# Optimization experiments

Measured on AMD Instinct MI355X. Metric: run time of the kernel, lower is better.

## Reference

```python
import jax, jax.numpy as jnp
import numpy as np

N, E, D, H = 16000, 256000, 128, 4
ALPHA = 0.2  # LeakyReLU negative slope


def setup_inputs() -> dict:
    key = jax.random.key(0)
    ks = jax.random.split(key, 9)
    s = 0.1
    return {
        "h": jax.random.normal(ks[0], (N, D), jnp.float32),
        "W": jax.random.normal(ks[1], (H, D, D), jnp.float32) * s,
        "a": jax.random.normal(ks[2], (H, 2 * D), jnp.float32) * s,
        "W_ih": jax.random.normal(ks[3], (3 * D, H * D), jnp.float32) * s,
        "W_hh": jax.random.normal(ks[4], (3 * D, D), jnp.float32) * s,
        "b_ih": jnp.zeros((3 * D,), jnp.float32),
        "b_hh": jnp.zeros((3 * D,), jnp.float32),
        "src": jax.random.randint(ks[5], (E,), 0, N, jnp.int32),
        "dst": jax.random.randint(ks[6], (E,), 0, N, jnp.int32),
    }


def reference(h, W, a, W_ih, W_hh, b_ih, b_hh, src, dst):
    n = h.shape[0]
    # Per-head linear transform: Wh[n,h,d]
    Wh = jnp.einsum("nd,hde->nhe", h, W)
    a1, a2 = a[:, :D], a[:, D:]
    s_src = jnp.einsum("nhd,hd->nh", Wh, a1)  # src attention logits
    s_dst = jnp.einsum("nhd,hd->nh", Wh, a2)  # dst attention logits
    e = jax.nn.leaky_relu(s_src[src] + s_dst[dst], ALPHA)  # [E,H]
    # Segment softmax over incoming edges of each dst node
    m = jax.ops.segment_max(e, dst, num_segments=n)          # [N,H]
    ex = jnp.exp(e - m[dst])
    denom = jax.ops.segment_sum(ex, dst, num_segments=n)     # [N,H]
    att = ex / denom[dst]                                    # [E,H]
    # Weighted message aggregation: h_prime[n,h,d]
    h_prime = jax.ops.segment_sum(att[:, :, None] * Wh[src], dst, num_segments=n)
    x = h_prime.reshape(n, H * D)  # concat heads
    # PyTorch GRUCell(input=H*D, hidden=D)
    gi = x @ W_ih.T + b_ih
    gh = h @ W_hh.T + b_hh
    i_r, i_z, i_n = jnp.split(gi, 3, axis=1)
    h_r, h_z, h_n = jnp.split(gh, 3, axis=1)
    r = jax.nn.sigmoid(i_r + h_r)
    z = jax.nn.sigmoid(i_z + h_z)
    nvec = jnp.tanh(i_n + r * h_n)
    return (1.0 - z) * nvec + z * h
```

## Files before the change

### kernel.cpp

```cpp
#include <hip/hip_runtime.h>
#include <math.h>

#define N_NODES 16000
#define E_EDGES 256000
#define DIM 128
#define HEADS 4
#define LRELU_ALPHA 0.2f
#define SLOT 64

typedef unsigned short u16;
typedef unsigned int u32;
typedef short bf16x8 __attribute__((ext_vector_type(8)));
typedef float floatx4 __attribute__((ext_vector_type(4)));

#define AS1 __attribute__((address_space(1)))
#define AS3 __attribute__((address_space(3)))

__device__ __forceinline__ u16 f2bf(float f) {
    u32 u = __float_as_uint(f);
    u32 r = (u + 0x7fffu + ((u >> 16) & 1u)) >> 16;
    return (u16)r;
}
__device__ __forceinline__ float bflo(u32 v) { return __uint_as_float(v << 16); }
__device__ __forceinline__ float bfhi(u32 v) { return __uint_as_float(v & 0xffff0000u); }
__device__ __forceinline__ float bfs(u16 v) { return __uint_as_float((u32)v << 16); }
__device__ __forceinline__ u32 pack2(float lo, float hi) {
    return (u32)f2bf(lo) | ((u32)f2bf(hi) << 16);
}


__device__ __forceinline__ void mt_tile(const float* __restrict__ W_ih,
    const float* __restrict__ W, u16* __restrict__ Wcat, int y, int z, char* SMp, int tid)
{
    u16 (*Alds)[32] = (u16(*)[32])SMp;
    u16 (*Blds)[32] = (u16(*)[32])(SMp + 8192);
    const int wave = tid >> 6;
    const int lane = tid & 63;
    const int quad = lane >> 4;
    const int l15  = lane & 15;
    const int wm = (wave >> 1) * 64;
    const int wn = (wave & 1) * 64;
    const int jrow = tid >> 1;
    const int eh = (tid & 1) * 16;

    floatx4 acc[4][4] = {};

    for (int k0 = 0; k0 < 128; k0 += 32) {
        const float* arow = W_ih + (size_t)(y * 128 + jrow) * 512 + z * 128 + k0 + eh;
        const float* brow = W + (size_t)(z * 128 + jrow) * 128 + k0 + eh;
        #pragma unroll
        for (int i = 0; i < 16; ++i) {
            Alds[jrow][eh + i] = f2bf(arow[i]);
            Blds[jrow][eh + i] = f2bf(brow[i]);
        }
        __syncthreads();
        bf16x8 af[4], bfr[4];
        #pragma unroll
        for (int i = 0; i < 4; ++i) af[i] = *(const bf16x8*)&Alds[wm + i * 16 + l15][quad * 8];
        #pragma unroll
        for (int j = 0; j < 4; ++j) bfr[j] = *(const bf16x8*)&Blds[wn + j * 16 + l15][quad * 8];
        #pragma unroll
        for (int i = 0; i < 4; ++i)
            #pragma unroll
            for (int j = 0; j < 4; ++j)
                acc[i][j] = __builtin_amdgcn_mfma_f32_16x16x32_bf16(af[i], bfr[j], acc[i][j], 0, 0, 0);
        __syncthreads();
    }
    u16* C = Wcat + z * 128;
    #pragma unroll
    for (int i = 0; i < 4; ++i) {
        #pragma unroll
        for (int r = 0; r < 4; ++r) {
            int row = y * 128 + wm + i * 16 + quad * 4 + r;
            int p = (row & 127) * 4 + (row >> 7);
            size_t base = (size_t)p * 640 + wn + l15;
            #pragma unroll
            for (int j = 0; j < 4; ++j) C[base + j * 16] = f2bf(acc[i][j][r]);
        }
    }
}

__global__ __launch_bounds__(256) void prep_kernel(
    const float* __restrict__ W, const float* __restrict__ a,
    const float* __restrict__ W_ih, const float* __restrict__ W_hh,
    const int* __restrict__ src, const int* __restrict__ dst,
    u16* __restrict__ Wcat, float* __restrict__ wa1, float* __restrict__ wa2,
    u32* __restrict__ cnt, int* __restrict__ ssort)
{
    __shared__ __align__(16) char SM[16384];
    const int b = blockIdx.x;
    const int tid = threadIdx.x;
    if (b < 1000) {
        int e = b * 256 + tid;
        u32 base = cnt[N_NODES];
        int d = dst[e];
        u32 pos = atomicAdd(&cnt[d], 1u) - base;
        ssort[d * SLOT + pos] = src[e];
    } else if (b < 1192) {
        int t = (b - 1000) * 256 + tid;
        int jp = t >> 7, e = t & 127;
        int gate = jp >> 7;
        if (gate == 2) gate = 3;
        int p = (jp & 127) * 4 + gate;
        Wcat[(size_t)p * 640 + 512 + e] = f2bf(W_hh[jp * 128 + e]);
    } else if (b < 1512) {
        int t = (b - 1192) * 256 + tid;
        if (t < 16384) {
            int d = t >> 7, e = t & 127;
            Wcat[(size_t)(d * 4 + 2) * 640 + 512 + e] = 0;
        } else {
            int t2 = t - 16384;
            int d = t2 >> 9, c = t2 & 511;
            Wcat[(size_t)(d * 4 + 3) * 640 + c] = 0;
        }
    } else if (b < 1514) {
        int t = (b - 1512) * 256 + tid;
        int h = t >> 7;
        const float* wrow = W + (long)t * DIM;
        const float* a1 = a + h * 2 * DIM;
        const float* a2 = a1 + DIM;
        float s1 = 0.f, s2 = 0.f;
        for (int e = 0; e < DIM; ++e) {
            float w = wrow[e];
            s1 = fmaf(w, a1[e], s1);
            s2 = fmaf(w, a2[e], s2);
        }
        wa1[t] = s1;
        wa2[t] = s2;
    } else {
        int t = b - 1514;
        mt_tile(W_ih, W, Wcat, t % 3, t / 3, SM, tid);
    }
}

__global__ __launch_bounds__(256) void scores_kernel(
    const float* __restrict__ hin, const float* __restrict__ wa1, const float* __restrict__ wa2,
    float* __restrict__ s_src, float* __restrict__ s_dst, u16* __restrict__ xcat)
{
    const int tid = threadIdx.x;
    const int lane = tid & 63;
    const int n = blockIdx.x * 4 + (tid >> 6);
    for (int nn = n; nn < N_NODES; nn += 4000) {
        float2 hv = ((const float2*)hin)[nn * 64 + lane];
        ((u32*)xcat)[nn * 320 + 256 + lane] = pack2(hv.x, hv.y);
        float ps[4], qs[4];
        #pragma unroll
        for (int h = 0; h < 4; ++h) {
            float2 w1 = ((const float2*)(wa1 + h * 128))[lane];
            float2 w2 = ((const float2*)(wa2 + h * 128))[lane];
            float p = hv.x * w1.x + hv.y * w1.y;
            float q = hv.x * w2.x + hv.y * w2.y;
            #pragma unroll
            for (int off = 32; off > 0; off >>= 1) {
                p += __shfl_xor(p, off, 64);
                q += __shfl_xor(q, off, 64);
            }
            ps[h] = p; qs[h] = q;
        }
        if (lane == 0) {
            #pragma unroll
            for (int h = 0; h < 4; ++h) {
                s_src[nn * HEADS + h] = ps[h];
                s_dst[nn * HEADS + h] = qs[h];
            }
        }
    }
}

__global__ __launch_bounds__(256) void aggregate_kernel(
    const float* __restrict__ s_src, const float* __restrict__ s_dst,
    const u32* __restrict__ cnt, const int* __restrict__ srcs,
    u16* __restrict__ xcat)
{
    const int tid = threadIdx.x;
    const int lane = tid & 63;
    const int n = blockIdx.x * 4 + (tid >> 6);
    const u32 base = cnt[N_NODES];
    const int deg = (int)(cnt[n] - base);
    const int start = n * SLOT;
    u32* xrow = (u32*)(xcat + (size_t)n * 640);
    if (deg == 0) {
        #pragma unroll
        for (int h = 0; h < 4; ++h) xrow[h * 64 + lane] = 0u;
        return;
    }
    const u32* hb = (const u32*)xcat;
    const float sd = s_dst[n * HEADS + (lane & 3)];
    const int j16 = lane >> 2;
    const int hh  = lane & 3;

    float2 acc[4] = {{0.f,0.f},{0.f,0.f},{0.f,0.f},{0.f,0.f}};
    float dsum[4] = {0.f, 0.f, 0.f, 0.f};

    for (int cb = 0; cb < deg; cb += 16) {
        const int clen = min(16, deg - cb);
        int sv = 0;
        if (lane < clen) sv = srcs[start + cb + lane];
        float wv = 0.f;
        if (j16 < clen) {
            int s = __shfl(sv, j16, 64);
            float e = s_src[s * HEADS + hh] + sd;
            e = e > 0.f ? e : LRELU_ALPHA * e;
            wv = __expf(e);
        }
        int e = 0;
        for (; e + 8 <= clen; e += 8) {
            u32 vs[8];
            #pragma unroll
            for (int k = 0; k < 8; ++k) {
                int s = __shfl(sv, e + k, 64);
                vs[k] = hb[s * 320 + 256 + lane];
            }
            #pragma unroll
            for (int k = 0; k < 8; ++k) {
                float lo = bflo(vs[k]), hi = bfhi(vs[k]);
                #pragma unroll
                for (int h = 0; h < 4; ++h) {
                    float w = __shfl(wv, (e + k) * 4 + h, 64);
                    acc[h].x = fmaf(w, lo, acc[h].x);
                    acc[h].y = fmaf(w, hi, acc[h].y);
                    dsum[h] += w;
                }
            }
        }
        for (; e < clen; ++e) {
            int s = __shfl(sv, e, 64);
            u32 v = hb[s * 320 + 256 + lane];
            float lo = bflo(v), hi = bfhi(v);
            #pragma unroll
            for (int h = 0; h < 4; ++h) {
                float w = __shfl(wv, e * 4 + h, 64);
                acc[h].x = fmaf(w, lo, acc[h].x);
                acc[h].y = fmaf(w, hi, acc[h].y);
                dsum[h] += w;
            }
        }
    }
    #pragma unroll
    for (int h = 0; h < 4; ++h) {
        float invd = 1.f / dsum[h];
        xrow[h * 64 + lane] = pack2(acc[h].x * invd, acc[h].y * invd);
    }
}

__global__ __launch_bounds__(256) void gemm_gru_kernel(
    const u16* __restrict__ xcat, const u16* __restrict__ Wcat,
    const float* __restrict__ b_ih, const float* __restrict__ b_hh,
    const float* __restrict__ hin, float* __restrict__ out)
{
    __shared__ __align__(16) char SM[32768];
    u16 (*Alds)[32] = (u16(*)[32])SM;
    u16 (*Blds)[32] = (u16(*)[32])(SM + 16384);
    u16 (*tile)[128] = (u16(*)[128])SM;
    const int tid = threadIdx.x;
    const int wave = tid >> 6;
    const int lane = tid & 63;
    const int quad = lane >> 4;
    const int l15  = lane & 15;
    const int row0 = blockIdx.y * 128;
    const int col0 = blockIdx.x * 128;
    const int wm = (wave >> 1) * 64;
    const int wn = (wave & 1) * 64;
    const int ch0 = wave * 2;
    const int srow = lane >> 2;
    const int scol = (lane & 3) * 8;

    floatx4 acc[4][4] = {};

    for (int k0 = 0; k0 < 640; k0 += 64) {
        #pragma unroll
        for (int kh = 0; kh < 2; ++kh) {
            #pragma unroll
            for (int c = 0; c < 2; ++c) {
                int ch = ch0 + c;
                const u16* ga = xcat + (size_t)(row0 + ch * 16 + srow) * 640 + k0 + kh * 32 + scol;
                __builtin_amdgcn_global_load_lds((AS1 void*)ga, (AS3 void*)&Alds[kh * 128 + ch * 16][0], 16, 0, 0);
                const u16* gb = Wcat + (size_t)(col0 + ch * 16 + srow) * 640 + k0 + kh * 32 + scol;
                __builtin_amdgcn_global_load_lds((AS1 void*)gb, (AS3 void*)&Blds[kh * 128 + ch * 16][0], 16, 0, 0);
            }
        }
        __syncthreads();
        #pragma unroll
        for (int kh = 0; kh < 2; ++kh) {
            bf16x8 af[4], bfr[4];
            #pragma unroll
            for (int i = 0; i < 4; ++i) af[i] = *(const bf16x8*)&Alds[kh * 128 + wm + i * 16 + l15][quad * 8];
            #pragma unroll
            for (int j = 0; j < 4; ++j) bfr[j] = *(const bf16x8*)&Blds[kh * 128 + wn + j * 16 + l15][quad * 8];
            #pragma unroll
            for (int i = 0; i < 4; ++i)
                #pragma unroll
                for (int j = 0; j < 4; ++j)
                    acc[i][j] = __builtin_amdgcn_mfma_f32_16x16x32_bf16(af[i], bfr[j], acc[i][j], 0, 0, 0);
        }
        __syncthreads();
    }
    #pragma unroll
    for (int i = 0; i < 4; ++i)
        #pragma unroll
        for (int r = 0; r < 4; ++r) {
            int row = wm + i * 16 + quad * 4 + r;
            #pragma unroll
            for (int j = 0; j < 4; ++j)
                tile[row][wn + j * 16 + l15] = f2bf(acc[i][j][r]);
        }
    __syncthreads();
    const int dim_l = tid & 31;
    const int rg = tid >> 5;
    const int dim_g = col0 / 4 + dim_l;
    const float bir = b_ih[dim_g],       bhr = b_hh[dim_g];
    const float biz = b_ih[128 + dim_g], bhz = b_hh[128 + dim_g];
    const float bin = b_ih[256 + dim_g], bhn = b_hh[256 + dim_g];
    #pragma unroll
    for (int i = 0; i < 16; ++i) {
        int row = rg * 16 + i;
        int node = row0 + row;
        ushort4 gv = *(const ushort4*)&tile[row][dim_l * 4];
        float A  = bfs(gv.x) + bir + bhr;
        float B  = bfs(gv.y) + biz + bhz;
        float Cn = bfs(gv.z) + bin;
        float Dn = bfs(gv.w) + bhn;
        float r = 1.f / (1.f + __expf(-A));
        float z = 1.f / (1.f + __expf(-B));
        float e2 = __expf(2.f * (Cn + r * Dn));
        float nv = (e2 - 1.f) / (e2 + 1.f);
        out[(size_t)node * 128 + dim_g] = (1.f - z) * nv + z * hin[(size_t)node * 128 + dim_g];
    }
}

extern "C" void kernel_launch(void* const* d_in, const int* in_sizes, int n_in,
                              void* d_out, int out_size, void* d_ws, size_t ws_size,
                              hipStream_t stream)
{
    const float* h    = (const float*)d_in[0];
    const float* W    = (const float*)d_in[1];
    const float* a    = (const float*)d_in[2];
    const float* W_ih = (const float*)d_in[3];
    const float* W_hh = (const float*)d_in[4];
    const float* b_ih = (const float*)d_in[5];
    const float* b_hh = (const float*)d_in[6];
    const int*   src  = (const int*)d_in[7];
    const int*   dst  = (const int*)d_in[8];
    float* out = (float*)d_out;

    char* ws = (char*)d_ws;
    size_t off = 0;
    auto alloc = [&](size_t bytes) { void* p = ws + off; off += (bytes + 255) & ~(size_t)255; return p; };

    u16*   xcat = (u16*)alloc((size_t)N_NODES * 640 * 2);
    u16*   Wcat = (u16*)alloc(512 * 640 * 2);
    float* wa1  = (float*)alloc(512 * 4);
    float* wa2  = (float*)alloc(512 * 4);
    float* s_src = (float*)alloc((size_t)N_NODES * HEADS * 4);
    float* s_dst = (float*)alloc((size_t)N_NODES * HEADS * 4);
    u32*   cnt  = (u32*)alloc((N_NODES + 1) * 4);
    int*   ssort = (int*)alloc((size_t)N_NODES * SLOT * 4);

    prep_kernel<<<1526, 256, 0, stream>>>(
        W, a, W_ih, W_hh, src, dst, Wcat, wa1, wa2, cnt, ssort);

    scores_kernel<<<1000, 256, 0, stream>>>(h, wa1, wa2, s_src, s_dst, xcat);

    aggregate_kernel<<<N_NODES / 4, 256, 0, stream>>>(s_src, s_dst, cnt, ssort, xcat);

    gemm_gru_kernel<<<dim3(4, 125), 256, 0, stream>>>(xcat, Wcat, b_ih, b_hh, h, out);
}
```

Baseline: 142.2 us.

## Merge prep, scores and aggregate into two kernels, recomputing W·a per block

Reorganises the first three launches into two. The edge scatter and node score computation now share one kernel, and each score block recomputes the W·a vectors into shared memory instead of reading them from a prior launch. The Wcat weight preparation (W_hh copy, zero fill, W_ih·W tiles) moves into the aggregation kernel as extra trailing blocks. This removes one launch and a kernel boundary, at the cost of redundant W·a work in 500 blocks and aggregation blocks sharing the GPU with weight-prep blocks.

```diff
diff --git a/kernel.cpp b/kernel.cpp
--- a/kernel.cpp
+++ b/kernel.cpp
@@ -28,6 +28,70 @@
     return (u32)f2bf(lo) | ((u32)f2bf(hi) << 16);
 }
 
+
+__global__ __launch_bounds__(256) void scatter_scores_kernel(
+    const float* __restrict__ hin, const float* __restrict__ W, const float* __restrict__ a,
+    const int* __restrict__ src, const int* __restrict__ dst,
+    float* __restrict__ s_src, float* __restrict__ s_dst, u16* __restrict__ xcat,
+    u32* __restrict__ cnt, int* __restrict__ ssort)
+{
+    __shared__ float wa1s[512];
+    __shared__ float wa2s[512];
+    const int b = blockIdx.x;
+    const int tid = threadIdx.x;
+    if (b < 1000) {
+        int e = b * 256 + tid;
+        u32 base = cnt[N_NODES];
+        int d = dst[e];
+        u32 pos = atomicAdd(&cnt[d], 1u) - base;
+        ssort[d * SLOT + pos] = src[e];
+        return;
+    }
+    for (int idx = tid; idx < 512; idx += 256) {
+        int h = idx >> 7;
+        const float4* wrow = (const float4*)(W + (size_t)idx * DIM);
+        const float4* a1 = (const float4*)(a + h * 2 * DIM);
+        const float4* a2 = (const float4*)(a + h * 2 * DIM + DIM);
+        float s1 = 0.f, s2 = 0.f;
+        for (int e4 = 0; e4 < 32; ++e4) {
+            float4 w = wrow[e4], x1 = a1[e4], x2 = a2[e4];
+            s1 = fmaf(w.x, x1.x, s1); s2 = fmaf(w.x, x2.x, s2);
+            s1 = fmaf(w.y, x1.y, s1); s2 = fmaf(w.y, x2.y, s2);
+            s1 = fmaf(w.z, x1.z, s1); s2 = fmaf(w.z, x2.z, s2);
+            s1 = fmaf(w.w, x1.w, s1); s2 = fmaf(w.w, x2.w, s2);
+        }
+        wa1s[idx] = s1;
+        wa2s[idx] = s2;
+    }
+    __syncthreads();
+    const int lane = tid & 63;
+    const int n0 = (b - 1000) * 4 + (tid >> 6);
+    for (int nn = n0; nn < N_NODES; nn += 2000) {
+        float2 hv = ((const float2*)hin)[nn * 64 + lane];
+        ((u32*)xcat)[nn * 320 + 256 + lane] = pack2(hv.x, hv.y);
+        float ps[4], qs[4];
+        #pragma unroll
+        for (int h = 0; h < 4; ++h) {
+            float2 w1 = ((const float2*)(wa1s + h * 128))[lane];
+            float2 w2 = ((const float2*)(wa2s + h * 128))[lane];
+            float p = hv.x * w1.x + hv.y * w1.y;
+            float q = hv.x * w2.x + hv.y * w2.y;
+            #pragma unroll
+            for (int off = 32; off > 0; off >>= 1) {
+                p += __shfl_xor(p, off, 64);
+                q += __shfl_xor(q, off, 64);
+            }
+            ps[h] = p; qs[h] = q;
+        }
+        if (lane == 0) {
+            #pragma unroll
+            for (int h = 0; h < 4; ++h) {
+                s_src[nn * HEADS + h] = ps[h];
+                s_dst[nn * HEADS + h] = qs[h];
+            }
+        }
+    }
+}
 
 __device__ __forceinline__ void mt_tile(const float* __restrict__ W_ih,
     const float* __restrict__ W, u16* __restrict__ Wcat, int y, int z, char* SMp, int tid)
@@ -80,101 +144,43 @@
     }
 }
 
-__global__ __launch_bounds__(256) void prep_kernel(
-    const float* __restrict__ W, const float* __restrict__ a,
-    const float* __restrict__ W_ih, const float* __restrict__ W_hh,
-    const int* __restrict__ src, const int* __restrict__ dst,
-    u16* __restrict__ Wcat, float* __restrict__ wa1, float* __restrict__ wa2,
-    u32* __restrict__ cnt, int* __restrict__ ssort)
+__global__ __launch_bounds__(256) void agg_wcat_kernel(
+    const float* __restrict__ s_src, const float* __restrict__ s_dst,
+    const u32* __restrict__ cnt, const int* __restrict__ srcs,
+    u16* __restrict__ xcat,
+    const float* __restrict__ W, const float* __restrict__ W_ih, const float* __restrict__ W_hh,
+    u16* __restrict__ Wcat)
 {
     __shared__ __align__(16) char SM[16384];
     const int b = blockIdx.x;
     const int tid = threadIdx.x;
-    if (b < 1000) {
-        int e = b * 256 + tid;
-        u32 base = cnt[N_NODES];
-        int d = dst[e];
-        u32 pos = atomicAdd(&cnt[d], 1u) - base;
-        ssort[d * SLOT + pos] = src[e];
-    } else if (b < 1192) {
-        int t = (b - 1000) * 256 + tid;
-        int jp = t >> 7, e = t & 127;
-        int gate = jp >> 7;
-        if (gate == 2) gate = 3;
-        int p = (jp & 127) * 4 + gate;
-        Wcat[(size_t)p * 640 + 512 + e] = f2bf(W_hh[jp * 128 + e]);
-    } else if (b < 1512) {
-        int t = (b - 1192) * 256 + tid;
-        if (t < 16384) {
-            int d = t >> 7, e = t & 127;
-            Wcat[(size_t)(d * 4 + 2) * 640 + 512 + e] = 0;
+    if (b >= 4000) {
+        int q = b - 4000;
+        if (q < 192) {
+            int t = q * 256 + tid;
+            int jp = t >> 7, e = t & 127;
+            int gate = jp >> 7;
+            if (gate == 2) gate = 3;
+            int p = (jp & 127) * 4 + gate;
+            Wcat[(size_t)p * 640 + 512 + e] = f2bf(W_hh[jp * 128 + e]);
+        } else if (q < 512) {
+            int t = (q - 192) * 256 + tid;
+            if (t < 16384) {
+                int d = t >> 7, e = t & 127;
+                Wcat[(size_t)(d * 4 + 2) * 640 + 512 + e] = 0;
+            } else {
+                int t2 = t - 16384;
+                int d = t2 >> 9, c = t2 & 511;
+                Wcat[(size_t)(d * 4 + 3) * 640 + c] = 0;
+            }
         } else {
-            int t2 = t - 16384;
-            int d = t2 >> 9, c = t2 & 511;
-            Wcat[(size_t)(d * 4 + 3) * 640 + c] = 0;
-        }
-    } else if (b < 1514) {
-        int t = (b - 1512) * 256 + tid;
-        int h = t >> 7;
-        const float* wrow = W + (long)t * DIM;
-        const float* a1 = a + h * 2 * DIM;
-        const float* a2 = a1 + DIM;
-        float s1 = 0.f, s2 = 0.f;
-        for (int e = 0; e < DIM; ++e) {
-            float w = wrow[e];
-            s1 = fmaf(w, a1[e], s1);
-            s2 = fmaf(w, a2[e], s2);
-        }
-        wa1[t] = s1;
-        wa2[t] = s2;
-    } else {
-        int t = b - 1514;
-        mt_tile(W_ih, W, Wcat, t % 3, t / 3, SM, tid);
-    }
-}
-
-__global__ __launch_bounds__(256) void scores_kernel(
-    const float* __restrict__ hin, const float* __restrict__ wa1, const float* __restrict__ wa2,
-    float* __restrict__ s_src, float* __restrict__ s_dst, u16* __restrict__ xcat)
-{
-    const int tid = threadIdx.x;
+            int t = q - 512;
+            mt_tile(W_ih, W, Wcat, t % 3, t / 3, SM, tid);
+        }
+        return;
+    }
     const int lane = tid & 63;
-    const int n = blockIdx.x * 4 + (tid >> 6);
-    for (int nn = n; nn < N_NODES; nn += 4000) {
-        float2 hv = ((const float2*)hin)[nn * 64 + lane];
-        ((u32*)xcat)[nn * 320 + 256 + lane] = pack2(hv.x, hv.y);
-        float ps[4], qs[4];
-        #pragma unroll
-        for (int h = 0; h < 4; ++h) {
-            float2 w1 = ((const float2*)(wa1 + h * 128))[lane];
-            float2 w2 = ((const float2*)(wa2 + h * 128))[lane];
-            float p = hv.x * w1.x + hv.y * w1.y;
-            float q = hv.x * w2.x + hv.y * w2.y;
-            #pragma unroll
-            for (int off = 32; off > 0; off >>= 1) {
-                p += __shfl_xor(p, off, 64);
-                q += __shfl_xor(q, off, 64);
-            }
-            ps[h] = p; qs[h] = q;
-        }
-        if (lane == 0) {
-            #pragma unroll
-            for (int h = 0; h < 4; ++h) {
-                s_src[nn * HEADS + h] = ps[h];
-                s_dst[nn * HEADS + h] = qs[h];
-            }
-        }
-    }
-}
-
-__global__ __launch_bounds__(256) void aggregate_kernel(
-    const float* __restrict__ s_src, const float* __restrict__ s_dst,
-    const u32* __restrict__ cnt, const int* __restrict__ srcs,
-    u16* __restrict__ xcat)
-{
-    const int tid = threadIdx.x;
-    const int lane = tid & 63;
-    const int n = blockIdx.x * 4 + (tid >> 6);
+    const int n = b * 4 + (tid >> 6);
     const u32 base = cnt[N_NODES];
     const int deg = (int)(cnt[n] - base);
     const int start = n * SLOT;
@@ -349,19 +355,16 @@
 
     u16*   xcat = (u16*)alloc((size_t)N_NODES * 640 * 2);
     u16*   Wcat = (u16*)alloc(512 * 640 * 2);
-    float* wa1  = (float*)alloc(512 * 4);
-    float* wa2  = (float*)alloc(512 * 4);
     float* s_src = (float*)alloc((size_t)N_NODES * HEADS * 4);
     float* s_dst = (float*)alloc((size_t)N_NODES * HEADS * 4);
     u32*   cnt  = (u32*)alloc((N_NODES + 1) * 4);
     int*   ssort = (int*)alloc((size_t)N_NODES * SLOT * 4);
 
-    prep_kernel<<<1526, 256, 0, stream>>>(
-        W, a, W_ih, W_hh, src, dst, Wcat, wa1, wa2, cnt, ssort);
-
-    scores_kernel<<<1000, 256, 0, stream>>>(h, wa1, wa2, s_src, s_dst, xcat);
-
-    aggregate_kernel<<<N_NODES / 4, 256, 0, stream>>>(s_src, s_dst, cnt, ssort, xcat);
+    scatter_scores_kernel<<<1500, 256, 0, stream>>>(
+        h, W, a, src, dst, s_src, s_dst, xcat, cnt, ssort);
+
+    agg_wcat_kernel<<<4524, 256, 0, stream>>>(
+        s_src, s_dst, cnt, ssort, xcat, W, W_ih, W_hh, Wcat);
 
     gemm_gru_kernel<<<dim3(4, 125), 256, 0, stream>>>(xcat, Wcat, b_ih, b_hh, h, out);
 }
```

Result: slower. 202.3 us (+42.2%).
